# Kernel optimization log

Hardware: AMD Instinct MI355X
Metric: run time of the kernel (lower is better)

The kernel has to match this reference:

```python
import jax, jax.numpy as jnp
import numpy as np

HID = 256
POS_FREQ = 10
DIR_FREQ = 4
POS_ENC = 3 * (2 * POS_FREQ + 1)   # 63
DIR_ENC = 3 * (2 * DIR_FREQ + 1)   # 27
N_PTS = 262144


def _posenc(x, num_freq):
    freqs = (2.0 ** jnp.arange(num_freq)).astype(x.dtype)      # [F]
    xf = x[..., None, :] * freqs[:, None]                       # [..., F, D]
    sc = jnp.stack([jnp.sin(xf), jnp.cos(xf)], axis=-2)         # [..., F, 2, D]
    return jnp.concatenate([x, sc.reshape(*x.shape[:-1], -1)], axis=-1)


def _linear_init(key, fan_in, fan_out):
    kw, kb = jax.random.split(key)
    s = 1.0 / np.sqrt(fan_in)
    W = jax.random.uniform(kw, (fan_in, fan_out), jnp.float32, -s, s)
    b = jax.random.uniform(kb, (fan_out,), jnp.float32, -s, s)
    return W, b


def setup_inputs() -> dict:
    key = jax.random.key(0)
    ks = jax.random.split(key, 16)
    inp = {
        "positions": jax.random.normal(ks[0], (N_PTS, 3), jnp.float32),
        "directions": jax.random.normal(ks[1], (N_PTS, 3), jnp.float32),
    }
    W, b = _linear_init(ks[2], POS_ENC, HID)
    inp["W_in"], inp["b_in"] = W, b
    # 7 hidden layers; layer index 4 takes skip concat (HID + POS_ENC)
    for i in range(7):
        fan_in = HID + POS_ENC if i == 4 else HID
        W, b = _linear_init(ks[3 + i], fan_in, HID)
        inp[f"W_h{i}"], inp[f"b_h{i}"] = W, b
    W, b = _linear_init(ks[10], HID, HID + 1)
    inp["W_out"], inp["b_out"] = W, b
    W, b = _linear_init(ks[11], HID + DIR_ENC, HID // 2)
    inp["W_r1"], inp["b_r1"] = W, b
    W, b = _linear_init(ks[12], HID // 2, 3)
    inp["W_r2"], inp["b_r2"] = W, b
    return inp


def _forward(positions, directions, W_in, b_in, hidden_params, W_out, b_out,
             W_r1, b_r1, W_r2, b_r2):
    pe = _posenc(positions, POS_FREQ)    # [N, 63]
    de = _posenc(directions, DIR_FREQ)   # [N, 27]
    h = jax.nn.relu(pe @ W_in + b_in)    # [N, 256]
    for i, (W, b) in enumerate(hidden_params):
        if i == 4:
            h = jnp.concatenate([h, pe], axis=-1)  # skip connection [N, 319]
        h = jax.nn.relu(h @ W + b)
    out = h @ W_out + b_out                      # [N, 257]
    features = out[..., :HID]                    # [N, 256]
    density = jax.nn.relu(out[..., HID:HID + 1])  # [N, 1]
    rgb_in = jnp.concatenate([features, de], axis=-1)  # [N, 283]
    rgb = jax.nn.sigmoid(jax.nn.relu(rgb_in @ W_r1 + b_r1) @ W_r2 + b_r2)  # [N, 3]
    return rgb, density


def reference(positions, directions, W_in, b_in,
              W_h0, b_h0, W_h1, b_h1, W_h2, b_h2, W_h3, b_h3,
              W_h4, b_h4, W_h5, b_h5, W_h6, b_h6,
              W_out, b_out, W_r1, b_r1, W_r2, b_r2):
    hidden = [(W_h0, b_h0), (W_h1, b_h1), (W_h2, b_h2), (W_h3, b_h3),
              (W_h4, b_h4), (W_h5, b_h5), (W_h6, b_h6)]
    return _forward(positions, directions, W_in, b_in, hidden,
                    W_out, b_out, W_r1, b_r1, W_r2, b_r2)
```

## Files before the change

kernel.cpp:

```cpp
#include <hip/hip_runtime.h>
#include <math.h>

#define NPTS 262144
#define MT 64

typedef __attribute__((ext_vector_type(8))) short bf16x8;
typedef __attribute__((ext_vector_type(4))) float f32x4;
typedef __attribute__((ext_vector_type(2))) unsigned int u32x2;

#if defined(__has_builtin)
#if __has_builtin(__builtin_amdgcn_cvt_pk_bf16_f32)
#define HAVE_CVT_PK_BF16 1
#endif
#endif

__device__ __forceinline__ short f2bf(float f) {
    union { float f; unsigned u; } v; v.f = f;
    unsigned r = v.u + 0x7fffu + ((v.u >> 16) & 1u);
    return (short)(r >> 16);
}
__device__ __forceinline__ unsigned pk2(float a, float b) {
#ifdef HAVE_CVT_PK_BF16
    auto r = __builtin_amdgcn_cvt_pk_bf16_f32(a, b);
    unsigned u; __builtin_memcpy(&u, &r, 4);
    return u;
#else
    return ((unsigned)(unsigned short)f2bf(a)) |
           ((unsigned)(unsigned short)f2bf(b) << 16);
#endif
}

#define OFF_IN   0
#define SZ_IN    (64*256)
#define OFF_H0   (OFF_IN + SZ_IN)
#define SZ_H     (256*256)
#define OFF_H1   (OFF_H0 + SZ_H)
#define OFF_H2   (OFF_H1 + SZ_H)
#define OFF_H3   (OFF_H2 + SZ_H)
#define OFF_H4   (OFF_H3 + SZ_H)
#define SZ_H4    (320*256)
#define OFF_H5   (OFF_H4 + SZ_H4)
#define OFF_H6   (OFF_H5 + SZ_H)
#define OFF_OUT  (OFF_H6 + SZ_H)
#define SZ_OUT   (256*272)
#define OFF_R1   (OFF_OUT + SZ_OUT)
#define SZ_R1    (288*128)
#define OFF_R2   (OFF_R1 + SZ_R1)
#define SZ_R2    (128*16)
#define WS_TOTAL (OFF_R2 + SZ_R2)

struct PrepP { const float* W[11]; short* ws; };

__global__ __launch_bounds__(256) void prep_all(PrepP pp) {
    int i = blockIdx.x * 256 + threadIdx.x;
    if (i >= WS_TOTAL) return;
    const int offs[12] = {OFF_IN, OFF_H0, OFF_H1, OFF_H2, OFF_H3, OFF_H4,
                          OFF_H5, OFF_H6, OFF_OUT, OFF_R1, OFF_R2, WS_TOTAL};
    const int Ks[11]  = {63,256,256,256,256,319,256,256,256,283,128};
    const int Ns[11]  = {256,256,256,256,256,256,256,256,257,128,3};
    const int Nps[11] = {256,256,256,256,256,256,256,256,272,128,16};
    int seg = 0;
    while (i >= offs[seg + 1]) seg++;
    int li = i - offs[seg];
    int j = li & 7, L = (li >> 3) & 63, tile = li >> 9;
    int nNt = Nps[seg] >> 4;
    int nt = tile % nNt, kt = tile / nNt;
    int k = kt * 32 + ((L >> 4) << 3) + j;
    int n = nt * 16 + (L & 15);
    float v = (k < Ks[seg] && n < Ns[seg]) ? pp.W[seg][k * Ns[seg] + n] : 0.f;
    pp.ws[i] = f2bf(v);
}

struct Params {
    const float *pos, *dir;
    const float *b_in, *b_h0, *b_h1, *b_h2, *b_h3, *b_h4, *b_h5, *b_h6;
    const float *b_out, *b_r1, *b_r2;
    const short *w;
    float *out;
};

template<int NKT, int NT, int NS, int MODE>
__device__ __forceinline__ void layerT(const short* __restrict__ Wsw,
                                       const float* __restrict__ bias,
                                       const short* Xin, short* Xout,
                                       float* dout, int p0,
                                       int ntB, int wave, int lane) {
    const int l15 = lane & 15, quad = lane >> 4;
    const short* xb = Xin + quad * 512 + l15 * 8;
    const short* wp = Wsw + (size_t)(ntB * 64 + lane) * 8;

    bf16x8 a0[NS], a1[NS];
#pragma unroll
    for (int s = 0; s < NS; s++)
        a0[s] = *(const bf16x8*)(wp + (size_t)s * 512);
    if (NKT > 1)
#pragma unroll
        for (int s = 0; s < NS; s++)
            a1[s] = *(const bf16x8*)(wp + (size_t)NT * 512 + s * 512);

    __syncthreads();

    if (MODE == 1 && wave < 4) {
        f32x4 ad = (f32x4){0.f, 0.f, 0.f, 0.f};
#pragma unroll
        for (int kt = 0; kt < NKT; ++kt) {
            bf16x8 b = *(const bf16x8*)(xb + wave * 128 + kt * 2048);
            bf16x8 a = *(const bf16x8*)(Wsw + (size_t)((kt * NT + 16) * 64 + lane) * 8);
            ad = __builtin_amdgcn_mfma_f32_16x16x32_bf16(a, b, ad, 0, 0, 0);
        }
        if (quad == 0)
            dout[3 * NPTS + p0 + wave * 16 + l15] = fmaxf(ad[0] + bias[256], 0.f);
    }

    f32x4 acc[NS][4];
#pragma unroll
    for (int s = 0; s < NS; s++)
#pragma unroll
        for (int t = 0; t < 4; t++) acc[s][t] = (f32x4){0.f, 0.f, 0.f, 0.f};

    bf16x8 b_c[4];
#pragma unroll
    for (int t = 0; t < 4; t++)
        b_c[t] = *(const bf16x8*)(xb + t * 128);

#pragma unroll
    for (int kt = 0; kt < NKT; ++kt) {
        bf16x8 b_n[4], a_n[NS];
        if (kt + 1 < NKT) {
#pragma unroll
            for (int t = 0; t < 4; t++)
                b_n[t] = *(const bf16x8*)(xb + (kt + 1) * 2048 + t * 128);
        }
        if (kt + 2 < NKT) {
#pragma unroll
            for (int s = 0; s < NS; s++)
                a_n[s] = *(const bf16x8*)(wp + (size_t)(kt + 2) * NT * 512 + s * 512);
        }
        if ((kt & 1) == 0) {
#pragma unroll
            for (int s = 0; s < NS; s++)
#pragma unroll
                for (int t = 0; t < 4; t++)
                    acc[s][t] = __builtin_amdgcn_mfma_f32_16x16x32_bf16(a0[s], b_c[t], acc[s][t], 0, 0, 0);
        } else {
#pragma unroll
            for (int s = 0; s < NS; s++)
#pragma unroll
                for (int t = 0; t < 4; t++)
                    acc[s][t] = __builtin_amdgcn_mfma_f32_16x16x32_bf16(a1[s], b_c[t], acc[s][t], 0, 0, 0);
        }
        if (kt + 2 < NKT) {
            if ((kt & 1) == 0) {
#pragma unroll
                for (int s = 0; s < NS; s++) a0[s] = a_n[s];
            } else {
#pragma unroll
                for (int s = 0; s < NS; s++) a1[s] = a_n[s];
            }
        }
        if (kt + 1 < NKT) {
#pragma unroll
            for (int t = 0; t < 4; t++) b_c[t] = b_n[t];
        }
    }

#pragma unroll
    for (int s = 0; s < NS; s++) {
        const int n0 = (ntB + s) * 16 + quad * 4;
        const f32x4 bv = *(const f32x4*)(bias + n0);
        short* xo = Xout + (2 * (ntB + s) + (quad >> 1)) * 512 + (quad & 1) * 4;
#pragma unroll
        for (int t = 0; t < 4; t++) {
            const int m = t * 16 + l15;
            float v0 = acc[s][t][0] + bv[0];
            float v1 = acc[s][t][1] + bv[1];
            float v2 = acc[s][t][2] + bv[2];
            float v3 = acc[s][t][3] + bv[3];
            if (MODE == 0) {
                v0 = fmaxf(v0, 0.f); v1 = fmaxf(v1, 0.f);
                v2 = fmaxf(v2, 0.f); v3 = fmaxf(v3, 0.f);
            }
            u32x2 w; w[0] = pk2(v0, v1); w[1] = pk2(v2, v3);
            *(u32x2*)(xo + m * 8) = w;
        }
    }
}

__global__ __launch_bounds__(512, 4) void nerf_fused(Params P) {
    __shared__ __align__(16) short XA[32 * 512];
    __shared__ __align__(16) short XB[40 * 512];
    const int tid = threadIdx.x;
    const int wave = tid >> 6, lane = tid & 63;
    const int p0 = blockIdx.x * MT;

    const int ntB_h = wave * 2;

    {
        const int pt = tid & 63, g = tid >> 6;
        const float x0 = P.pos[(p0 + pt) * 3 + 0];
        const float x1 = P.pos[(p0 + pt) * 3 + 1];
        const float x2 = P.pos[(p0 + pt) * 3 + 2];
        bf16x8 v;
#pragma unroll
        for (int j = 0; j < 8; j++) {
            const int d = g * 8 + j;
            float val = 0.f;
            if (d < 3) val = (d == 0) ? x0 : (d == 1) ? x1 : x2;
            else if (d < 63) {
                const int e = d - 3, f = e / 6, r = e % 6;
                const float x = (r % 3 == 0) ? x0 : (r % 3 == 1) ? x1 : x2;
                const float xf = x * (float)(1 << f);
                val = (r < 3) ? sinf(xf) : cosf(xf);
            }
            v[j] = f2bf(val);
        }
        *(bf16x8*)(XA + ((size_t)g * 64 + pt) * 8) = v;
        *(bf16x8*)(XB + ((size_t)(32 + g) * 64 + pt) * 8) = v;
    }

    bf16x8 de_v;
    if (wave < 4) {
        const int pt = tid & 63, g = wave;
        const float x0 = P.dir[(p0 + pt) * 3 + 0];
        const float x1 = P.dir[(p0 + pt) * 3 + 1];
        const float x2 = P.dir[(p0 + pt) * 3 + 2];
#pragma unroll
        for (int j = 0; j < 8; j++) {
            const int d = g * 8 + j;
            float val = 0.f;
            if (d < 3) val = (d == 0) ? x0 : (d == 1) ? x1 : x2;
            else if (d < 27) {
                const int e = d - 3, f = e / 6, r = e % 6;
                const float x = (r % 3 == 0) ? x0 : (r % 3 == 1) ? x1 : x2;
                const float xf = x * (float)(1 << f);
                val = (r < 3) ? sinf(xf) : cosf(xf);
            }
            de_v[j] = f2bf(val);
        }
    }

    layerT<2, 16, 2, 0>(P.w + OFF_IN, P.b_in, XA, XB, P.out, p0, ntB_h, wave, lane);
    layerT<8, 16, 2, 0>(P.w + OFF_H0, P.b_h0, XB, XA, P.out, p0, ntB_h, wave, lane);
    layerT<8, 16, 2, 0>(P.w + OFF_H1, P.b_h1, XA, XB, P.out, p0, ntB_h, wave, lane);
    layerT<8, 16, 2, 0>(P.w + OFF_H2, P.b_h2, XB, XA, P.out, p0, ntB_h, wave, lane);
    layerT<8, 16, 2, 0>(P.w + OFF_H3, P.b_h3, XA, XB, P.out, p0, ntB_h, wave, lane);
    layerT<10, 16, 2, 0>(P.w + OFF_H4, P.b_h4, XB, XA, P.out, p0, ntB_h, wave, lane);
    layerT<8, 16, 2, 0>(P.w + OFF_H5, P.b_h5, XA, XB, P.out, p0, ntB_h, wave, lane);

    if (wave < 4)
        *(bf16x8*)(XB + ((size_t)(32 + wave) * 64 + (tid & 63)) * 8) = de_v;

    layerT<8, 16, 2, 0>(P.w + OFF_H6, P.b_h6, XB, XA, P.out, p0, ntB_h, wave, lane);
    layerT<8, 17, 2, 1>(P.w + OFF_OUT, P.b_out, XA, XB, P.out, p0, ntB_h, wave, lane);

    layerT<9, 8, 1, 0>(P.w + OFF_R1, P.b_r1, XB, XA, P.out, p0, wave, wave, lane);

    __syncthreads();
    if (wave < 4) {
        const int l15 = lane & 15, quad = lane >> 4;
        f32x4 acc = (f32x4){0.f, 0.f, 0.f, 0.f};
        const short* xb = XA + quad * 512 + (wave * 16 + l15) * 8;
#pragma unroll
        for (int kt = 0; kt < 4; ++kt) {
            bf16x8 b = *(const bf16x8*)(xb + kt * 2048);
            bf16x8 a = *(const bf16x8*)(P.w + OFF_R2 + (size_t)(kt * 64 + lane) * 8);
            acc = __builtin_amdgcn_mfma_f32_16x16x32_bf16(a, b, acc, 0, 0, 0);
        }
        if (quad == 0) {
#pragma unroll
            for (int r = 0; r < 3; r++) {
                const float v = acc[r] + P.b_r2[r];
                P.out[(size_t)(p0 + wave * 16 + l15) * 3 + r] = 1.f / (1.f + expf(-v));
            }
        }
    }
}

extern "C" void kernel_launch(void* const* d_in, const int* in_sizes, int n_in,
                              void* d_out, int out_size, void* d_ws, size_t ws_size,
                              hipStream_t stream) {
    short* ws = (short*)d_ws;

    PrepP pp;
    pp.W[0]  = (const float*)d_in[2];
    pp.W[1]  = (const float*)d_in[4];
    pp.W[2]  = (const float*)d_in[6];
    pp.W[3]  = (const float*)d_in[8];
    pp.W[4]  = (const float*)d_in[10];
    pp.W[5]  = (const float*)d_in[12];
    pp.W[6]  = (const float*)d_in[14];
    pp.W[7]  = (const float*)d_in[16];
    pp.W[8]  = (const float*)d_in[18];
    pp.W[9]  = (const float*)d_in[20];
    pp.W[10] = (const float*)d_in[22];
    pp.ws = ws;
    hipLaunchKernelGGL(prep_all, dim3((WS_TOTAL + 255) / 256), dim3(256), 0, stream, pp);

    Params P;
    P.pos  = (const float*)d_in[0];
    P.dir  = (const float*)d_in[1];
    P.b_in = (const float*)d_in[3];
    P.b_h0 = (const float*)d_in[5];
    P.b_h1 = (const float*)d_in[7];
    P.b_h2 = (const float*)d_in[9];
    P.b_h3 = (const float*)d_in[11];
    P.b_h4 = (const float*)d_in[13];
    P.b_h5 = (const float*)d_in[15];
    P.b_h6 = (const float*)d_in[17];
    P.b_out = (const float*)d_in[19];
    P.b_r1 = (const float*)d_in[21];
    P.b_r2 = (const float*)d_in[23];
    P.w = ws;
    P.out = (float*)d_out;
    hipLaunchKernelGGL(nerf_fused, dim3(NPTS / MT), dim3(512), 0, stream, P);
}
```

Measured before the change: 409.4 us.

## Switch MLP layers from 16x16x32 to 32x32x16 MFMA tiles

Replaces the 16x16x32 bf16 MFMA layer routine with one built on 32x32x16 MFMA. Each wave now owns a 32-column output block across 64 points, and the weight prep kernel emits a matching swizzled layout. The density column of the output layer moves into its own small 16x16 weight segment. The larger MFMA tile is meant to halve A-operand register loads and instruction count per FLOP, at the cost of a different LDS access pattern and new layout bookkeeping with possible bank conflicts.

```diff
diff --git a/kernel.cpp b/kernel.cpp
--- a/kernel.cpp
+++ b/kernel.cpp
@@ -6,6 +6,7 @@
 
 typedef __attribute__((ext_vector_type(8))) short bf16x8;
 typedef __attribute__((ext_vector_type(4))) float f32x4;
+typedef __attribute__((ext_vector_type(16))) float f32x16;
 typedef __attribute__((ext_vector_type(2))) unsigned int u32x2;
 
 #if defined(__has_builtin)
@@ -42,8 +43,10 @@
 #define OFF_H5   (OFF_H4 + SZ_H4)
 #define OFF_H6   (OFF_H5 + SZ_H)
 #define OFF_OUT  (OFF_H6 + SZ_H)
-#define SZ_OUT   (256*272)
-#define OFF_R1   (OFF_OUT + SZ_OUT)
+#define SZ_OUTM  (256*256)
+#define OFF_OUTD (OFF_OUT + SZ_OUTM)
+#define SZ_OUTD  (256*16)
+#define OFF_R1   (OFF_OUTD + SZ_OUTD)
 #define SZ_R1    (288*128)
 #define OFF_R2   (OFF_R1 + SZ_R1)
 #define SZ_R2    (128*16)
@@ -54,20 +57,32 @@
 __global__ __launch_bounds__(256) void prep_all(PrepP pp) {
     int i = blockIdx.x * 256 + threadIdx.x;
     if (i >= WS_TOTAL) return;
-    const int offs[12] = {OFF_IN, OFF_H0, OFF_H1, OFF_H2, OFF_H3, OFF_H4,
-                          OFF_H5, OFF_H6, OFF_OUT, OFF_R1, OFF_R2, WS_TOTAL};
-    const int Ks[11]  = {63,256,256,256,256,319,256,256,256,283,128};
-    const int Ns[11]  = {256,256,256,256,256,256,256,256,257,128,3};
-    const int Nps[11] = {256,256,256,256,256,256,256,256,272,128,16};
+    const int offs[13] = {OFF_IN, OFF_H0, OFF_H1, OFF_H2, OFF_H3, OFF_H4,
+                          OFF_H5, OFF_H6, OFF_OUT, OFF_OUTD, OFF_R1, OFF_R2,
+                          WS_TOTAL};
+    const int wsrc[12] = {0,1,2,3,4,5,6,7,8,8,9,10};
+    const int Ks[12]   = {63,256,256,256,256,319,256,256,256,256,283,128};
+    const int Nsrc[12] = {256,256,256,256,256,256,256,256,257,257,128,3};
     int seg = 0;
     while (i >= offs[seg + 1]) seg++;
     int li = i - offs[seg];
     int j = li & 7, L = (li >> 3) & 63, tile = li >> 9;
-    int nNt = Nps[seg] >> 4;
-    int nt = tile % nNt, kt = tile / nNt;
-    int k = kt * 32 + ((L >> 4) << 3) + j;
-    int n = nt * 16 + (L & 15);
-    float v = (k < Ks[seg] && n < Ns[seg]) ? pp.W[seg][k * Ns[seg] + n] : 0.f;
+    const float* W = pp.W[wsrc[seg]];
+    float v = 0.f;
+    if (seg == 9) {
+        int k = tile * 32 + ((L >> 4) << 3) + j;
+        if (k < 256 && (L & 15) == 0) v = W[k * 257 + 256];
+    } else if (seg == 11) {
+        int k = tile * 32 + ((L >> 4) << 3) + j;
+        int n = L & 15;
+        if (k < 128 && n < 3) v = W[k * 3 + n];
+    } else {
+        int nNb = (seg == 10) ? 4 : 8;
+        int nb = tile % nNb, kt = tile / nNb;
+        int k = kt * 16 + ((L >> 5) << 3) + j;
+        int n = nb * 32 + (L & 31);
+        if (k < Ks[seg]) v = W[k * Nsrc[seg] + n];
+    }
     pp.ws[i] = f2bf(v);
 }
 
@@ -79,109 +94,92 @@
     float *out;
 };
 
-template<int NKT, int NT, int NS, int MODE>
-__device__ __forceinline__ void layerT(const short* __restrict__ Wsw,
-                                       const float* __restrict__ bias,
-                                       const short* Xin, short* Xout,
-                                       float* dout, int p0,
-                                       int ntB, int wave, int lane) {
-    const int l15 = lane & 15, quad = lane >> 4;
-    const short* xb = Xin + quad * 512 + l15 * 8;
-    const short* wp = Wsw + (size_t)(ntB * 64 + lane) * 8;
-
-    bf16x8 a0[NS], a1[NS];
-#pragma unroll
-    for (int s = 0; s < NS; s++)
-        a0[s] = *(const bf16x8*)(wp + (size_t)s * 512);
-    if (NKT > 1)
-#pragma unroll
-        for (int s = 0; s < NS; s++)
-            a1[s] = *(const bf16x8*)(wp + (size_t)NT * 512 + s * 512);
+template<int NKT, int NNB, int TM, int MODE>
+__device__ __forceinline__ void layer32(const short* __restrict__ Wsw,
+                                        const short* __restrict__ Wd,
+                                        const float* __restrict__ bias,
+                                        const short* Xin, short* Xout,
+                                        float* dout, int p0,
+                                        int nb, int mbB, int wave, int lane) {
+    const int l31 = lane & 31, hi = lane >> 5;
+    const short* xb = Xin + hi * 512 + l31 * 8 + mbB * 256;
+    const short* wp = Wsw + (size_t)(nb * 64 + lane) * 8;
+
+    bf16x8 a0 = *(const bf16x8*)(wp);
+    bf16x8 a1 = *(const bf16x8*)(wp + (size_t)NNB * 512);
 
     __syncthreads();
 
     if (MODE == 1 && wave < 4) {
+        const int l15 = lane & 15, quad = lane >> 4;
+        const short* xd = Xin + quad * 512 + (wave * 16 + l15) * 8;
         f32x4 ad = (f32x4){0.f, 0.f, 0.f, 0.f};
 #pragma unroll
-        for (int kt = 0; kt < NKT; ++kt) {
-            bf16x8 b = *(const bf16x8*)(xb + wave * 128 + kt * 2048);
-            bf16x8 a = *(const bf16x8*)(Wsw + (size_t)((kt * NT + 16) * 64 + lane) * 8);
+        for (int kt = 0; kt < 8; ++kt) {
+            bf16x8 b = *(const bf16x8*)(xd + kt * 2048);
+            bf16x8 a = *(const bf16x8*)(Wd + (size_t)(kt * 64 + lane) * 8);
             ad = __builtin_amdgcn_mfma_f32_16x16x32_bf16(a, b, ad, 0, 0, 0);
         }
         if (quad == 0)
             dout[3 * NPTS + p0 + wave * 16 + l15] = fmaxf(ad[0] + bias[256], 0.f);
     }
 
-    f32x4 acc[NS][4];
-#pragma unroll
-    for (int s = 0; s < NS; s++)
-#pragma unroll
-        for (int t = 0; t < 4; t++) acc[s][t] = (f32x4){0.f, 0.f, 0.f, 0.f};
-
-    bf16x8 b_c[4];
-#pragma unroll
-    for (int t = 0; t < 4; t++)
-        b_c[t] = *(const bf16x8*)(xb + t * 128);
+    f32x16 acc[TM];
+#pragma unroll
+    for (int t = 0; t < TM; t++)
+#pragma unroll
+        for (int r = 0; r < 16; r++) acc[t][r] = 0.f;
+
+    bf16x8 b_c[TM];
+#pragma unroll
+    for (int t = 0; t < TM; t++)
+        b_c[t] = *(const bf16x8*)(xb + t * 256);
 
 #pragma unroll
     for (int kt = 0; kt < NKT; ++kt) {
-        bf16x8 b_n[4], a_n[NS];
+        bf16x8 b_n[TM], a_n;
         if (kt + 1 < NKT) {
 #pragma unroll
-            for (int t = 0; t < 4; t++)
-                b_n[t] = *(const bf16x8*)(xb + (kt + 1) * 2048 + t * 128);
+            for (int t = 0; t < TM; t++)
+                b_n[t] = *(const bf16x8*)(xb + (kt + 1) * 1024 + t * 256);
+        }
+        if (kt + 2 < NKT)
+            a_n = *(const bf16x8*)(wp + (size_t)(kt + 2) * NNB * 512);
+        if ((kt & 1) == 0) {
+#pragma unroll
+            for (int t = 0; t < TM; t++)
+                acc[t] = __builtin_amdgcn_mfma_f32_32x32x16_bf16(a0, b_c[t], acc[t], 0, 0, 0);
+        } else {
+#pragma unroll
+            for (int t = 0; t < TM; t++)
+                acc[t] = __builtin_amdgcn_mfma_f32_32x32x16_bf16(a1, b_c[t], acc[t], 0, 0, 0);
         }
         if (kt + 2 < NKT) {
-#pragma unroll
-            for (int s = 0; s < NS; s++)
-                a_n[s] = *(const bf16x8*)(wp + (size_t)(kt + 2) * NT * 512 + s * 512);
-        }
-        if ((kt & 1) == 0) {
-#pragma unroll
-            for (int s = 0; s < NS; s++)
-#pragma unroll
-                for (int t = 0; t < 4; t++)
-                    acc[s][t] = __builtin_amdgcn_mfma_f32_16x16x32_bf16(a0[s], b_c[t], acc[s][t], 0, 0, 0);
-        } else {
-#pragma unroll
-            for (int s = 0; s < NS; s++)
-#pragma unroll
-                for (int t = 0; t < 4; t++)
-                    acc[s][t] = __builtin_amdgcn_mfma_f32_16x16x32_bf16(a1[s], b_c[t], acc[s][t], 0, 0, 0);
-        }
-        if (kt + 2 < NKT) {
-            if ((kt & 1) == 0) {
-#pragma unroll
-                for (int s = 0; s < NS; s++) a0[s] = a_n[s];
-            } else {
-#pragma unroll
-                for (int s = 0; s < NS; s++) a1[s] = a_n[s];
-            }
+            if ((kt & 1) == 0) a0 = a_n; else a1 = a_n;
         }
         if (kt + 1 < NKT) {
 #pragma unroll
-            for (int t = 0; t < 4; t++) b_c[t] = b_n[t];
-        }
-    }
-
-#pragma unroll
-    for (int s = 0; s < NS; s++) {
-        const int n0 = (ntB + s) * 16 + quad * 4;
-        const f32x4 bv = *(const f32x4*)(bias + n0);
-        short* xo = Xout + (2 * (ntB + s) + (quad >> 1)) * 512 + (quad & 1) * 4;
-#pragma unroll
-        for (int t = 0; t < 4; t++) {
-            const int m = t * 16 + l15;
-            float v0 = acc[s][t][0] + bv[0];
-            float v1 = acc[s][t][1] + bv[1];
-            float v2 = acc[s][t][2] + bv[2];
-            float v3 = acc[s][t][3] + bv[3];
+            for (int t = 0; t < TM; t++) b_c[t] = b_n[t];
+        }
+    }
+
+#pragma unroll
+    for (int t = 0; t < TM; t++) {
+        const int m = (mbB + t) * 32 + l31;
+#pragma unroll
+        for (int rq = 0; rq < 4; rq++) {
+            const int nbase = nb * 32 + rq * 8 + hi * 4;
+            const f32x4 bv = *(const f32x4*)(bias + nbase);
+            float v0 = acc[t][rq * 4 + 0] + bv[0];
+            float v1 = acc[t][rq * 4 + 1] + bv[1];
+            float v2 = acc[t][rq * 4 + 2] + bv[2];
+            float v3 = acc[t][rq * 4 + 3] + bv[3];
             if (MODE == 0) {
                 v0 = fmaxf(v0, 0.f); v1 = fmaxf(v1, 0.f);
                 v2 = fmaxf(v2, 0.f); v3 = fmaxf(v3, 0.f);
             }
             u32x2 w; w[0] = pk2(v0, v1); w[1] = pk2(v2, v3);
-            *(u32x2*)(xo + m * 8) = w;
+            *(u32x2*)(Xout + ((size_t)(nb * 4 + rq) * 64 + m) * 8 + hi * 4) = w;
         }
     }
 }
@@ -192,8 +190,6 @@
     const int tid = threadIdx.x;
     const int wave = tid >> 6, lane = tid & 63;
     const int p0 = blockIdx.x * MT;
-
-    const int ntB_h = wave * 2;
 
     {
         const int pt = tid & 63, g = tid >> 6;
@@ -239,21 +235,21 @@
         }
     }
 
-    layerT<2, 16, 2, 0>(P.w + OFF_IN, P.b_in, XA, XB, P.out, p0, ntB_h, wave, lane);
-    layerT<8, 16, 2, 0>(P.w + OFF_H0, P.b_h0, XB, XA, P.out, p0, ntB_h, wave, lane);
-    layerT<8, 16, 2, 0>(P.w + OFF_H1, P.b_h1, XA, XB, P.out, p0, ntB_h, wave, lane);
-    layerT<8, 16, 2, 0>(P.w + OFF_H2, P.b_h2, XB, XA, P.out, p0, ntB_h, wave, lane);
-    layerT<8, 16, 2, 0>(P.w + OFF_H3, P.b_h3, XA, XB, P.out, p0, ntB_h, wave, lane);
-    layerT<10, 16, 2, 0>(P.w + OFF_H4, P.b_h4, XB, XA, P.out, p0, ntB_h, wave, lane);
-    layerT<8, 16, 2, 0>(P.w + OFF_H5, P.b_h5, XA, XB, P.out, p0, ntB_h, wave, lane);
+    layer32< 4, 8, 2, 0>(P.w + OFF_IN, nullptr, P.b_in, XA, XB, P.out, p0, wave, 0, wave, lane);
+    layer32<16, 8, 2, 0>(P.w + OFF_H0, nullptr, P.b_h0, XB, XA, P.out, p0, wave, 0, wave, lane);
+    layer32<16, 8, 2, 0>(P.w + OFF_H1, nullptr, P.b_h1, XA, XB, P.out, p0, wave, 0, wave, lane);
+    layer32<16, 8, 2, 0>(P.w + OFF_H2, nullptr, P.b_h2, XB, XA, P.out, p0, wave, 0, wave, lane);
+    layer32<16, 8, 2, 0>(P.w + OFF_H3, nullptr, P.b_h3, XA, XB, P.out, p0, wave, 0, wave, lane);
+    layer32<20, 8, 2, 0>(P.w + OFF_H4, nullptr, P.b_h4, XB, XA, P.out, p0, wave, 0, wave, lane);
+    layer32<16, 8, 2, 0>(P.w + OFF_H5, nullptr, P.b_h5, XA, XB, P.out, p0, wave, 0, wave, lane);
 
     if (wave < 4)
         *(bf16x8*)(XB + ((size_t)(32 + wave) * 64 + (tid & 63)) * 8) = de_v;
 
-    layerT<8, 16, 2, 0>(P.w + OFF_H6, P.b_h6, XB, XA, P.out, p0, ntB_h, wave, lane);
-    layerT<8, 17, 2, 1>(P.w + OFF_OUT, P.b_out, XA, XB, P.out, p0, ntB_h, wave, lane);
-
-    layerT<9, 8, 1, 0>(P.w + OFF_R1, P.b_r1, XB, XA, P.out, p0, wave, wave, lane);
+    layer32<16, 8, 2, 0>(P.w + OFF_H6, nullptr, P.b_h6, XB, XA, P.out, p0, wave, 0, wave, lane);
+    layer32<16, 8, 2, 1>(P.w + OFF_OUT, P.w + OFF_OUTD, P.b_out, XA, XB, P.out, p0, wave, 0, wave, lane);
+
+    layer32<18, 4, 1, 0>(P.w + OFF_R1, nullptr, P.b_r1, XB, XA, P.out, p0, wave & 3, wave >> 2, wave, lane);
 
     __syncthreads();
     if (wave < 4) {
```

After: 437.9 us. 6.9% more time.
